# Performance work log

Hardware: AMD Instinct MI355X
Metric: run time of the kernel (lower is better)

## Reference

```python
import jax, jax.numpy as jnp
import numpy as np

B, W, G, E, NI, K = 2048, 8192, 8, 128, 16, 15


def setup_inputs() -> dict:
    key = jax.random.key(0)
    ks = jax.random.split(key, 12)
    wavelengths_nm = jnp.linspace(300.0, 400.0, W, dtype=jnp.float32)
    # Rayleigh optical depth (Hansen & Travis style approximation), AMF=1 column
    lam_um = wavelengths_nm / 1000.0
    rayleigh_od = (0.008569 * lam_um ** -4
                   * (1.0 + 0.0113 * lam_um ** -2 + 0.00013 * lam_um ** -4)).astype(jnp.float32)
    return {
        "gas_columns": jax.random.uniform(ks[0], (B, G), jnp.float32),
        "instrument_ids": jax.random.randint(ks[1], (B,), 0, NI),
        "nuisance_latent": jax.random.normal(ks[2], (B, G), jnp.float32),
        "air_mass": 1.0 + 2.0 * jax.random.uniform(ks[3], (B,), jnp.float32),
        "wavelengths_nm": wavelengths_nm,
        "absorption": 0.1 * jax.random.uniform(ks[4], (G, W), jnp.float32),
        "continuum_basis": 0.05 * jax.random.normal(ks[5], (G + 1, W), jnp.float32),
        "rayleigh_od": rayleigh_od,
        "embed_table": jax.random.normal(ks[6], (NI, E), jnp.float32),
        "w1": jax.random.normal(ks[7], (E + G, 64), jnp.float32) / np.sqrt(E + G),
        "b1": jnp.zeros((64,), jnp.float32),
        "w2": jax.random.normal(ks[8], (64, 7), jnp.float32) / 8.0,
        "b2": jnp.zeros((7,), jnp.float32),
    }


def _gaussian_kernel(width_px, kernel_size):
    half = (kernel_size - 1) / 2
    pos = jnp.linspace(-half, half, kernel_size, dtype=width_px.dtype)  # [K]
    k = jnp.exp(-0.5 * (pos[None, :] / (width_px[:, None] + 1e-6)) ** 2)  # [B,K]
    return k / k.sum(axis=1, keepdims=True)


def _forward(gas_columns, nuisance_latent, air_mass, wavelengths_nm, absorption,
             continuum_basis, rayleigh_od, embed_table, w1, b1, w2, b2,
             instrument_ids):
    b = gas_columns.shape[0]
    am = air_mass[:, None]                                   # [B,1]
    scaled = gas_columns * am                                # [B,G]
    optical_depth = scaled @ absorption                      # [B,W]
    ones = jnp.ones((b, 1), gas_columns.dtype)
    continuum = jnp.concatenate([gas_columns, ones], axis=1) @ continuum_basis  # [B,W]
    differential = optical_depth + continuum + am * rayleigh_od[None, :]

    # nuisance MLP on [latent, embedding]
    embed = embed_table[instrument_ids]                      # [B,E]
    nin = jnp.concatenate([nuisance_latent, embed], axis=-1)
    h = jax.nn.gelu(nin @ w1 + b1, approximate=False)
    p = h @ w2 + b2                                          # [B,7]

    gain = jax.nn.softplus(p[:, 0]) + 0.001
    offset = p[:, 1]
    woff = 0.05 * jnp.tanh(p[:, 2])
    wscale = 1.0 + 0.005 * jnp.tanh(p[:, 3])
    lsf = jnp.clip(jax.nn.softplus(p[:, 4]) + 0.001, 0.2, 5.0)
    stray = jax.nn.sigmoid(p[:, 5]) * 0.05
    nonlin = 0.02 * jnp.tanh(p[:, 6])

    # per-sample wavelength shift/scale + linear resampling
    new_wl = wavelengths_nm[None, :] * wscale[:, None] + woff[:, None]  # [B,W]
    differential = jax.vmap(lambda wq, d: jnp.interp(wq, wavelengths_nm, d))(new_wl, differential)

    # per-sample Gaussian LSF convolution (replicate padding)
    kernel = _gaussian_kernel(lsf, K)                        # [B,K]
    pad = K // 2
    padded = jnp.pad(differential, ((0, 0), (pad, pad)), mode='edge')  # [B,W+K-1]
    n = differential.shape[1]
    convolved = sum(padded[:, k:k + n] * kernel[:, k:k + 1] for k in range(K))

    counts = jnp.exp(-convolved)
    post = gain[:, None] * counts + offset[:, None]
    total_nl = jnp.clip(nonlin, -0.04, 0.04)                 # instrument nonlinearity = 0
    nl_counts = post + total_nl[:, None] * post ** 2
    total_stray = jnp.clip(stray, 0.0, 0.2)                  # instrument stray = 0
    simulated = (1.0 - total_stray[:, None]) * nl_counts \
        + total_stray[:, None] * nl_counts.mean(axis=1, keepdims=True)
    return simulated


def reference(gas_columns, instrument_ids, nuisance_latent, air_mass,
              wavelengths_nm, absorption, continuum_basis, rayleigh_od,
              embed_table, w1, b1, w2, b2):
    return _forward(gas_columns, nuisance_latent, air_mass, wavelengths_nm,
                    absorption, continuum_basis, rayleigh_od, embed_table,
                    w1, b1, w2, b2, instrument_ids)
```

## Files before the change

kernel.cpp:

```cpp
#include <hip/hip_runtime.h>

#define W_ 8192
#define NBATCH 2048
#define NT 256
#define NWAVE 4
#define SEGW 2048
#define CCH 256
#define NCHW 8
#define IRW 272

typedef unsigned short u16_t;
typedef _Float16 h2v __attribute__((ext_vector_type(2)));

__device__ __forceinline__ u16_t f2h(float x){ _Float16 h=(_Float16)x; return __builtin_bit_cast(u16_t,h); }
__device__ __forceinline__ float h2f(u16_t u){ return (float)__builtin_bit_cast(_Float16,u); }
__device__ __forceinline__ unsigned pk2(float a,float b){ return (unsigned)f2h(a)|((unsigned)f2h(b)<<16); }
__device__ __forceinline__ float dot2u(unsigned a,unsigned b,float c){
#if __has_builtin(__builtin_amdgcn_fdot2)
  return __builtin_amdgcn_fdot2(__builtin_bit_cast(h2v,a),__builtin_bit_cast(h2v,b),c,false);
#else
  h2v ha=__builtin_bit_cast(h2v,a), hb=__builtin_bit_cast(h2v,b);
  return c+(float)ha[0]*(float)hb[0]+(float)ha[1]*(float)hb[1];
#endif
}
__device__ __forceinline__ unsigned pkrtz(float a,float b){
#if __has_builtin(__builtin_amdgcn_cvt_pkrtz)
  return __builtin_bit_cast(unsigned, __builtin_amdgcn_cvt_pkrtz(a,b));
#else
  return pk2(a,b);
#endif
}
__device__ __forceinline__ unsigned alignb(unsigned hi, unsigned lo){
#if __has_builtin(__builtin_amdgcn_alignbit)
  return __builtin_amdgcn_alignbit(hi, lo, 16);
#else
  return (lo >> 16) | (hi << 16);
#endif
}
__device__ __forceinline__ float softplusf(float x){ return fmaxf(x,0.f)+log1pf(expf(-fabsf(x))); }
__device__ __forceinline__ unsigned rflv(unsigned v){
  return (unsigned)__builtin_amdgcn_readfirstlane((int)v);
}
__device__ __forceinline__ float rflvf(float v){
  return __builtin_bit_cast(float, __builtin_amdgcn_readfirstlane(__builtin_bit_cast(int, v)));
}

__global__ __launch_bounds__(256, 2)
void doas_pack(const float* __restrict__ absn, const float* __restrict__ cbn,
               const float* __restrict__ ray, unsigned* __restrict__ Tp){
  const int w = blockIdx.x*256 + threadIdx.x;
  #pragma unroll
  for (int q=0;q<4;++q) Tp[q*W_+w]     = pk2(absn[(2*q)*W_+w], absn[(2*q+1)*W_+w]);
  #pragma unroll
  for (int q=0;q<4;++q) Tp[(4+q)*W_+w] = pk2(cbn[(2*q)*W_+w],  cbn[(2*q+1)*W_+w]);
  Tp[8*W_+w] = pk2(cbn[8*W_+w], ray[w]);
}

template<bool CLO, bool CHI>
__device__ __forceinline__ void interp_chunk(int cbase, int l, const unsigned* __restrict__ rU,
                                             unsigned* __restrict__ irowU,
                                             float wscale, float posoff){
  #pragma unroll
  for (int it=0; it<3; ++it){
    const int pi = it*64 + l;
    if (pi < 136){
      float v2[2];
      #pragma unroll
      for (int u=0;u<2;++u){
        int j = cbase + 2*pi + u;
        if (CLO) j = max(j, 0);
        if (CHI) j = min(j, W_-1);
        float pos = fmaf((float)j, wscale, posoff);
        if (CLO) pos = fmaxf(pos, 0.0f);
        if (CHI) pos = fminf(pos, 8191.0f);
        int i0 = (int)pos;
        if (CHI) i0 = min(i0, W_-2);
        const float fr = pos - (float)i0;
        const int m = i0 >> 1;
        const unsigned u0 = rU[m];
        const unsigned u1 = rU[m+1];
        const unsigned hu0 = u0 >> 16;
        const bool odd = (i0 & 1);
        const unsigned ua = odd ? hu0 : u0;
        const unsigned ub = odd ? u1  : hu0;
        const float d0 = h2f((u16_t)ua);
        const float d1 = h2f((u16_t)ub);
        v2[u] = fmaf(fr, d1-d0, d0);
      }
      irowU[pi] = pkrtz(v2[0], v2[1]);
    }
  }
}

__global__ __launch_bounds__(NT, 2)
void doas_main9(const unsigned* __restrict__ Tp, const float* __restrict__ gas,
                const float* __restrict__ air, const int* __restrict__ iid,
                const float* __restrict__ nuis, const float* __restrict__ emb,
                const float* __restrict__ w1, const float* __restrict__ b1,
                const float* __restrict__ w2, const float* __restrict__ b2,
                float* __restrict__ out){
  __shared__ u16_t rowH[W_ + 16];
  __shared__ u16_t irowS[NWAVE][IRW];
  __shared__ float hS[64];
  __shared__ float pS[8];
  __shared__ float scalS[44];
  __shared__ float wsumS[NWAVE];

  const int tid = threadIdx.x;
  const int row = blockIdx.x;
  const int wid = tid >> 6, l = tid & 63;
  const int segbase = wid * SEGW;

  unsigned csg[9];
  {
    const float am = air[row];
    const float* gfp = gas + (size_t)row * 8;
    #pragma unroll
    for (int q=0;q<4;++q) csg[q]   = rflv(pk2(gfp[2*q]*am, gfp[2*q+1]*am));
    #pragma unroll
    for (int q=0;q<4;++q) csg[4+q] = rflv(pk2(gfp[2*q],    gfp[2*q+1]));
    csg[8] = rflv(pk2(1.0f, am));
  }

  unsigned* rowHU = (unsigned*)rowH;
  #pragma unroll
  for (int it=0; it<8; ++it){
    const int e0 = it*1024 + tid*4;
    uint4 dq[9];
    #pragma unroll
    for (int q=0;q<9;++q) dq[q] = *(const uint4*)(Tp + q*W_ + e0);
    float a0=0.f, a1=0.f, a2=0.f, a3=0.f;
    #pragma unroll
    for (int q=0;q<9;++q){
      a0 = dot2u(dq[q].x, csg[q], a0);
      a1 = dot2u(dq[q].y, csg[q], a1);
      a2 = dot2u(dq[q].z, csg[q], a2);
      a3 = dot2u(dq[q].w, csg[q], a3);
    }
    *(uint2*)(rowHU + (e0 >> 1)) = make_uint2(pkrtz(a0,a1), pkrtz(a2,a3));
  }

  if (tid < 64) {
    const int id = iid[row];
    float acc = b1[tid];
    const float* nrow = nuis + (size_t)row * 8;
    #pragma unroll
    for (int i = 0; i < 8; ++i) acc = fmaf(nrow[i], w1[i*64 + tid], acc);
    const float* erow = emb + (size_t)id * 128;
    #pragma unroll 8
    for (int i = 0; i < 128; ++i) acc = fmaf(erow[i], w1[(8+i)*64 + tid], acc);
    hS[tid] = 0.5f * acc * (1.0f + erff(acc * 0.70710678118654752f));
  }
  __syncthreads();
  if (tid < 7) {
    float p = b2[tid];
    for (int j = 0; j < 64; ++j) p = fmaf(hS[j], w2[j*7+tid], p);
    pS[tid] = p;
  }
  __syncthreads();
  if (tid == 0) {
    float p0=pS[0], p1=pS[1], p2=pS[2], p3=pS[3], p4=pS[4], p5=pS[5], p6=pS[6];
    float gainv = softplusf(p0) + 0.001f;
    float offv  = p1;
    float woffv = 0.05f * tanhf(p2);
    float wscv  = 1.0f + 0.005f * tanhf(p3);
    float lsf   = fminf(fmaxf(softplusf(p4) + 0.001f, 0.2f), 5.0f);
    float strv  = fminf(fmaxf((1.0f/(1.0f+expf(-p5))) * 0.05f, 0.0f), 0.2f);
    float nlin  = fminf(fmaxf(0.02f * tanhf(p6), -0.04f), 0.04f);
    float iw = 1.0f/(lsf + 1e-6f);
    float ks[15]; float ksum = 0.f;
    #pragma unroll
    for (int k2=0;k2<15;++k2){ float pp=(float)(k2-7)*iw; float e=expf(-0.5f*pp*pp); ks[k2]=e; ksum+=e; }
    float inv = 1.0f/ksum;
    unsigned* su = (unsigned*)scalS;
    #pragma unroll
    for (int i=0;i<7;++i) su[32+i] = pk2(ks[2*i]*inv, ks[2*i+1]*inv);
    su[39] = pk2(ks[14]*inv, 0.0f);
    scalS[15] = wscv;
    scalS[16] = (300.0f*(wscv - 1.0f) + woffv) * (8191.0f/100.0f);
    scalS[17] = gainv; scalS[18] = offv; scalS[19] = nlin; scalS[20] = strv;
  }
  __syncthreads();

  const unsigned* scalU = (const unsigned*)scalS;
  unsigned kwp[7];
  #pragma unroll
  for (int i=0;i<7;++i) kwp[i] = rflv(scalU[32+i]);
  const unsigned k14lo = rflv(scalU[39]);
  const float wscale = rflvf(scalS[15]), posoff = rflvf(scalS[16]);
  const float gainv  = rflvf(scalS[17]), offv   = rflvf(scalS[18]);
  const float nlin   = rflvf(scalS[19]), strv   = rflvf(scalS[20]);

  const unsigned* rU = (const unsigned*)rowH;
  u16_t* irow = &irowS[wid][0];
  unsigned* irowU = (unsigned*)irow;

  float accsum = 0.f;
  unsigned nlp[NCHW][2];

  #pragma unroll
  for (int c = 0; c < NCHW; ++c) {
    const int cs = segbase + c*CCH;
    const int cbase = cs - 8;
    if (wid == 0 && c == 0)
      interp_chunk<true,false>(cbase, l, rU, irowU, wscale, posoff);
    else if (wid == NWAVE-1 && c == NCHW-1)
      interp_chunk<false,true>(cbase, l, rU, irowU, wscale, posoff);
    else
      interp_chunk<false,false>(cbase, l, rU, irowU, wscale, posoff);
    __builtin_amdgcn_wave_barrier();
    {
      const uint2* p2 = (const uint2*)irowU + l;
      const uint2 A = p2[0], B = p2[1], C = p2[2], D = p2[3], E = p2[4];
      unsigned q[10] = {A.x,A.y, B.x,B.y, C.x,C.y, D.x,D.y, E.x,E.y};
      unsigned sh[9];
      #pragma unroll
      for (int m=0;m<9;++m) sh[m] = alignb(q[m+1], q[m]);
      float nlv[4];
      #pragma unroll
      for (int t=0;t<4;++t){
        float cv = 0.f;
        if ((t & 1) == 0){
          const int b0 = t >> 1;
          #pragma unroll
          for (int i=0;i<7;++i) cv = dot2u(sh[b0+i], kwp[i], cv);
          cv = dot2u(sh[b0+7], k14lo, cv);
        } else {
          const int b0 = (t+1) >> 1;
          #pragma unroll
          for (int i=0;i<7;++i) cv = dot2u(q[b0+i], kwp[i], cv);
          cv = dot2u(q[b0+7], k14lo, cv);
        }
        const float counts = __expf(-cv);
        const float post = fmaf(gainv, counts, offv);
        const float v = fmaf(nlin*post, post, post);
        accsum += v;
        nlv[t] = v;
      }
      nlp[c][0] = pkrtz(nlv[0], nlv[1]);
      nlp[c][1] = pkrtz(nlv[2], nlv[3]);
    }
    __builtin_amdgcn_wave_barrier();
  }

  float s = accsum;
  #pragma unroll
  for (int off2 = 32; off2 >= 1; off2 >>= 1) s += __shfl_down(s, off2);
  if (l == 0) wsumS[wid] = s;
  __syncthreads();
  const float meanv = (wsumS[0]+wsumS[1]+wsumS[2]+wsumS[3]) * (1.0f/8192.0f);

  {
    const float aa = 1.0f - strv;
    const float bb = strv * meanv;
    float* orow = out + (size_t)row * W_;
    #pragma unroll
    for (int c = 0; c < NCHW; ++c) {
      const unsigned u0 = nlp[c][0], u1 = nlp[c][1];
      float4 o0;
      o0.x = fmaf(aa, h2f((u16_t)(u0 & 0xffffu)), bb);
      o0.y = fmaf(aa, h2f((u16_t)(u0 >> 16)),     bb);
      o0.z = fmaf(aa, h2f((u16_t)(u1 & 0xffffu)), bb);
      o0.w = fmaf(aa, h2f((u16_t)(u1 >> 16)),     bb);
      *(float4*)(orow + segbase + c*CCH + 4*l) = o0;
    }
  }
}

__global__ __launch_bounds__(256, 2)
void doas_mono(const float* __restrict__ gas, const int* __restrict__ iid,
               const float* __restrict__ nuis, const float* __restrict__ air,
               const float* __restrict__ absn, const float* __restrict__ cbn,
               const float* __restrict__ ray, const float* __restrict__ emb,
               const float* __restrict__ w1, const float* __restrict__ b1,
               const float* __restrict__ w2, const float* __restrict__ b2,
               float* __restrict__ out)
{
  __shared__ u16_t ringS[4][2048];
  __shared__ u16_t irowS2[4][544];
  __shared__ float hS[64];
  __shared__ float pS[8];
  __shared__ float scalS[52];
  __shared__ float wsumS[4];

  const int tid = threadIdx.x;
  const int row = blockIdx.x;

  if (tid < 64) {
    const int j = tid;
    const int id = iid[row];
    float acc = b1[j];
    const float* nrow = nuis + (size_t)row * 8;
    #pragma unroll
    for (int i = 0; i < 8; ++i) acc = fmaf(nrow[i], w1[i*64 + j], acc);
    const float* erow = emb + (size_t)id * 128;
    for (int i = 0; i < 128; ++i) acc = fmaf(erow[i], w1[(8+i)*64 + j], acc);
    hS[j] = 0.5f * acc * (1.0f + erff(acc * 0.70710678118654752f));
  }
  __syncthreads();
  if (tid < 7) {
    float p = b2[tid];
    for (int j = 0; j < 64; ++j) p = fmaf(hS[j], w2[j*7+tid], p);
    pS[tid] = p;
  }
  __syncthreads();
  if (tid == 0) {
    float p0=pS[0], p1=pS[1], p2=pS[2], p3=pS[3], p4=pS[4], p5=pS[5], p6=pS[6];
    float gainv = softplusf(p0) + 0.001f;
    float offv  = p1;
    float woffv = 0.05f * tanhf(p2);
    float wscv  = 1.0f + 0.005f * tanhf(p3);
    float lsf   = fminf(fmaxf(softplusf(p4) + 0.001f, 0.2f), 5.0f);
    float strv  = fminf(fmaxf((1.0f/(1.0f+expf(-p5))) * 0.05f, 0.0f), 0.2f);
    float nlin  = fminf(fmaxf(0.02f * tanhf(p6), -0.04f), 0.04f);
    float iw = 1.0f/(lsf + 1e-6f);
    float ks[15]; float ksum = 0.f;
    #pragma unroll
    for (int k2=0;k2<15;++k2){ float pp=(float)(k2-7)*iw; float e=expf(-0.5f*pp*pp); ks[k2]=e; ksum+=e; }
    float inv = 1.0f/ksum;
    scalS[15] = wscv;
    scalS[16] = (300.0f*(wscv - 1.0f) + woffv) * (8191.0f/100.0f);
    scalS[17] = gainv; scalS[18] = offv; scalS[19] = nlin; scalS[20] = strv;
    scalS[22] = air[row];
    unsigned* su = (unsigned*)scalS;
    #pragma unroll
    for (int i=0;i<7;++i) su[32+i] = pk2(ks[2*i]*inv, ks[2*i+1]*inv);
    su[39] = pk2(ks[14]*inv, 0.0f);
    su[40] = pk2(0.0f, ks[14]*inv);
    #pragma unroll
    for (int g=0; g<8; ++g) scalS[23+g] = gas[(size_t)row*8+g];
  }
  __syncthreads();

  const int wid = tid >> 6, l = tid & 63;
  const int segbase = wid * 2048;
  const unsigned* scalU = (const unsigned*)scalS;
  unsigned kwp[7];
  #pragma unroll
  for (int i=0;i<7;++i) kwp[i] = rflv(scalU[32+i]);
  const unsigned k14lo = rflv(scalU[39]), k14hi = rflv(scalU[40]);
  const float wscale = scalS[15], posoff = scalS[16];
  const float gainv  = scalS[17], offv   = scalS[18];
  const float nlin   = scalS[19], strv   = scalS[20];

  u16_t* ring = &ringS[wid][0];
  unsigned* ringU = (unsigned*)ring;
  u16_t* irow = &irowS2[wid][0];
  unsigned* irowU = (unsigned*)irow;

  auto do_diff = [&](int s){
    const int sbase = segbase - 256 + (s << 9);
    #pragma unroll
    for (int it=0; it<4; ++it){
      const int e0 = sbase + ((it*64 + l) << 1);
      const int eL = min(max(e0, 0), W_-2);
      const float am = scalS[22];
      float a0=0.f, a1=0.f;
      #pragma unroll
      for (int g=0; g<8; ++g){
        const float cg = scalS[23+g];
        const float ca = cg*am;
        a0 = fmaf(ca, absn[g*W_+eL],   a0); a0 = fmaf(cg, cbn[g*W_+eL],   a0);
        a1 = fmaf(ca, absn[g*W_+eL+1], a1); a1 = fmaf(cg, cbn[g*W_+eL+1], a1);
      }
      a0 += cbn[8*W_+eL]   + am*ray[eL];
      a1 += cbn[8*W_+eL+1] + am*ray[eL+1];
      ringU[((unsigned)e0 & 2047) >> 1] = pkrtz(a0, a1);
    }
  };

  float accsum = 0.f;
  unsigned nlp[4][4];

  do_diff(0); do_diff(1);
  __builtin_amdgcn_wave_barrier();

  #pragma unroll
  for (int c = 0; c < 4; ++c) {
    if (c < 3) do_diff(c+2);
    __builtin_amdgcn_wave_barrier();
    {
      const int cbase = segbase + (c << 9) - 8;
      #pragma unroll
      for (int it = 0; it < 5; ++it) {
        const int pi = it*64 + l;
        if (pi < 264) {
          float v2[2];
          #pragma unroll
          for (int u=0; u<2; ++u){
            const int j = cbase + 2*pi + u;
            const int jc = min(max(j, 0), W_-1);
            float pos = fmaf((float)jc, wscale, posoff);
            pos = fminf(fmaxf(pos, 0.0f), 8191.0f);
            const int i0 = min((int)pos, W_-2);
            const float fr = pos - (float)i0;
            const float d0 = h2f(ring[ i0    & 2047]);
            const float d1 = h2f(ring[(i0+1) & 2047]);
            v2[u] = fmaf(fr, d1-d0, d0);
          }
          irowU[pi] = pkrtz(v2[0], v2[1]);
        }
      }
    }
    __builtin_amdgcn_wave_barrier();
    {
      const uint4* qp = (const uint4*)irow + l;
      const uint4 A = qp[0], B = qp[1], C = qp[2];
      unsigned q[12] = {A.x,A.y,A.z,A.w, B.x,B.y,B.z,B.w, C.x,C.y,C.z,C.w};
      unsigned sh[10];
      #pragma unroll
      for (int m=0;m<10;++m) sh[m] = alignb(q[m+1], q[m]);
      float nlv[8];
      #pragma unroll
      for (int t=0;t<8;++t){
        const int s2 = t >> 1;
        float cv = 0.f;
        if ((t & 1) == 0){
          #pragma unroll
          for (int i=0;i<7;++i) cv = dot2u(sh[s2+i], kwp[i], cv);
          cv = dot2u(q[s2+7], k14hi, cv);
        } else {
          #pragma unroll
          for (int i=0;i<7;++i) cv = dot2u(q[s2+1+i], kwp[i], cv);
          cv = dot2u(q[s2+8], k14lo, cv);
        }
        const float counts = __expf(-cv);
        const float post = fmaf(gainv, counts, offv);
        const float v = fmaf(nlin*post, post, post);
        accsum += v;
        nlv[t] = v;
      }
      nlp[c][0] = pkrtz(nlv[0], nlv[1]);
      nlp[c][1] = pkrtz(nlv[2], nlv[3]);
      nlp[c][2] = pkrtz(nlv[4], nlv[5]);
      nlp[c][3] = pkrtz(nlv[6], nlv[7]);
    }
    __builtin_amdgcn_wave_barrier();
  }

  float s = accsum;
  #pragma unroll
  for (int off2 = 32; off2 >= 1; off2 >>= 1) s += __shfl_down(s, off2);
  if (l == 0) wsumS[wid] = s;
  __syncthreads();
  const float meanv = (wsumS[0]+wsumS[1]+wsumS[2]+wsumS[3]) * (1.0f/8192.0f);

  {
    const float aa = 1.0f - strv;
    const float bb = strv * meanv;
    float* orow = out + (size_t)row * W_;
    #pragma unroll
    for (int c = 0; c < 4; ++c) {
      const unsigned u0 = nlp[c][0], u1 = nlp[c][1], u2 = nlp[c][2], u3 = nlp[c][3];
      float4 o0, o1;
      o0.x = fmaf(aa, h2f((u16_t)(u0 & 0xffffu)), bb);
      o0.y = fmaf(aa, h2f((u16_t)(u0 >> 16)),     bb);
      o0.z = fmaf(aa, h2f((u16_t)(u1 & 0xffffu)), bb);
      o0.w = fmaf(aa, h2f((u16_t)(u1 >> 16)),     bb);
      o1.x = fmaf(aa, h2f((u16_t)(u2 & 0xffffu)), bb);
      o1.y = fmaf(aa, h2f((u16_t)(u2 >> 16)),     bb);
      o1.z = fmaf(aa, h2f((u16_t)(u3 & 0xffffu)), bb);
      o1.w = fmaf(aa, h2f((u16_t)(u3 >> 16)),     bb);
      float* dst = orow + segbase + (c << 9) + 8*l;
      *(float4*)(dst)     = o0;
      *(float4*)(dst + 4) = o1;
    }
  }
}

extern "C" void kernel_launch(void* const* d_in, const int* in_sizes, int n_in,
                              void* d_out, int out_size, void* d_ws, size_t ws_size,
                              hipStream_t stream) {
  const float* gas  = (const float*)d_in[0];
  const int*   iid  = (const int*)d_in[1];
  const float* nuis = (const float*)d_in[2];
  const float* air  = (const float*)d_in[3];
  const float* wl   = (const float*)d_in[4];
  const float* absn = (const float*)d_in[5];
  const float* cbn  = (const float*)d_in[6];
  const float* ray  = (const float*)d_in[7];
  const float* emb  = (const float*)d_in[8];
  const float* w1   = (const float*)d_in[9];
  const float* b1   = (const float*)d_in[10];
  const float* w2   = (const float*)d_in[11];
  const float* b2   = (const float*)d_in[12];
  float* out = (float*)d_out;
  (void)in_sizes; (void)n_in; (void)out_size; (void)wl;

  const size_t packBytes = (size_t)9 * W_ * 4;

  if (ws_size >= packBytes) {
    unsigned* Tp = (unsigned*)d_ws;
    hipLaunchKernelGGL(doas_pack, dim3(W_/256), dim3(256), 0, stream, absn, cbn, ray, Tp);
    hipLaunchKernelGGL(doas_main9, dim3(NBATCH), dim3(NT), 0, stream,
                       Tp, gas, air, iid, nuis, emb, w1, b1, w2, b2, out);
  } else {
    hipLaunchKernelGGL(doas_mono, dim3(NBATCH), dim3(256), 0, stream,
                       gas, iid, nuis, air, absn, cbn, ray, emb, w1, b1, w2, b2, out);
  }
}
```

Before: 60.65 us.

## Specialize warps: three build spectrum row while fourth runs nuisance MLP

Splits the block by wavefront. Wavefronts 0-2 compute the optical-depth row (now 11 iterations of 768 elements, with a bounds check). Wavefront 3 concurrently computes the nuisance MLP and reduces the second layer with wave shuffles instead of shared memory. This removes two block-wide barriers and the serial second-layer loop, overlapping the MLP with the row build. The cost is that the row build runs on three wavefronts instead of four, and the last iteration is partially masked.

```diff
diff --git a/kernel.cpp b/kernel.cpp
--- a/kernel.cpp
+++ b/kernel.cpp
@@ -93,16 +93,14 @@
 }
 
 __global__ __launch_bounds__(NT, 2)
-void doas_main9(const unsigned* __restrict__ Tp, const float* __restrict__ gas,
-                const float* __restrict__ air, const int* __restrict__ iid,
-                const float* __restrict__ nuis, const float* __restrict__ emb,
-                const float* __restrict__ w1, const float* __restrict__ b1,
-                const float* __restrict__ w2, const float* __restrict__ b2,
-                float* __restrict__ out){
+void doas_main11(const unsigned* __restrict__ Tp, const float* __restrict__ gas,
+                 const float* __restrict__ air, const int* __restrict__ iid,
+                 const float* __restrict__ nuis, const float* __restrict__ emb,
+                 const float* __restrict__ w1, const float* __restrict__ b1,
+                 const float* __restrict__ w2, const float* __restrict__ b2,
+                 float* __restrict__ out){
   __shared__ u16_t rowH[W_ + 16];
   __shared__ u16_t irowS[NWAVE][IRW];
-  __shared__ float hS[64];
-  __shared__ float pS[8];
   __shared__ float scalS[44];
   __shared__ float wsumS[NWAVE];
 
@@ -111,74 +109,83 @@
   const int wid = tid >> 6, l = tid & 63;
   const int segbase = wid * SEGW;
 
-  unsigned csg[9];
-  {
-    const float am = air[row];
-    const float* gfp = gas + (size_t)row * 8;
-    #pragma unroll
-    for (int q=0;q<4;++q) csg[q]   = rflv(pk2(gfp[2*q]*am, gfp[2*q+1]*am));
-    #pragma unroll
-    for (int q=0;q<4;++q) csg[4+q] = rflv(pk2(gfp[2*q],    gfp[2*q+1]));
-    csg[8] = rflv(pk2(1.0f, am));
-  }
-
-  unsigned* rowHU = (unsigned*)rowH;
-  #pragma unroll
-  for (int it=0; it<8; ++it){
-    const int e0 = it*1024 + tid*4;
-    uint4 dq[9];
-    #pragma unroll
-    for (int q=0;q<9;++q) dq[q] = *(const uint4*)(Tp + q*W_ + e0);
-    float a0=0.f, a1=0.f, a2=0.f, a3=0.f;
-    #pragma unroll
-    for (int q=0;q<9;++q){
-      a0 = dot2u(dq[q].x, csg[q], a0);
-      a1 = dot2u(dq[q].y, csg[q], a1);
-      a2 = dot2u(dq[q].z, csg[q], a2);
-      a3 = dot2u(dq[q].w, csg[q], a3);
-    }
-    *(uint2*)(rowHU + (e0 >> 1)) = make_uint2(pkrtz(a0,a1), pkrtz(a2,a3));
-  }
-
-  if (tid < 64) {
-    const int id = iid[row];
-    float acc = b1[tid];
-    const float* nrow = nuis + (size_t)row * 8;
-    #pragma unroll
-    for (int i = 0; i < 8; ++i) acc = fmaf(nrow[i], w1[i*64 + tid], acc);
-    const float* erow = emb + (size_t)id * 128;
-    #pragma unroll 8
-    for (int i = 0; i < 128; ++i) acc = fmaf(erow[i], w1[(8+i)*64 + tid], acc);
-    hS[tid] = 0.5f * acc * (1.0f + erff(acc * 0.70710678118654752f));
-  }
-  __syncthreads();
-  if (tid < 7) {
-    float p = b2[tid];
-    for (int j = 0; j < 64; ++j) p = fmaf(hS[j], w2[j*7+tid], p);
-    pS[tid] = p;
-  }
-  __syncthreads();
-  if (tid == 0) {
-    float p0=pS[0], p1=pS[1], p2=pS[2], p3=pS[3], p4=pS[4], p5=pS[5], p6=pS[6];
-    float gainv = softplusf(p0) + 0.001f;
-    float offv  = p1;
-    float woffv = 0.05f * tanhf(p2);
-    float wscv  = 1.0f + 0.005f * tanhf(p3);
-    float lsf   = fminf(fmaxf(softplusf(p4) + 0.001f, 0.2f), 5.0f);
-    float strv  = fminf(fmaxf((1.0f/(1.0f+expf(-p5))) * 0.05f, 0.0f), 0.2f);
-    float nlin  = fminf(fmaxf(0.02f * tanhf(p6), -0.04f), 0.04f);
-    float iw = 1.0f/(lsf + 1e-6f);
-    float ks[15]; float ksum = 0.f;
-    #pragma unroll
-    for (int k2=0;k2<15;++k2){ float pp=(float)(k2-7)*iw; float e=expf(-0.5f*pp*pp); ks[k2]=e; ksum+=e; }
-    float inv = 1.0f/ksum;
-    unsigned* su = (unsigned*)scalS;
-    #pragma unroll
-    for (int i=0;i<7;++i) su[32+i] = pk2(ks[2*i]*inv, ks[2*i+1]*inv);
-    su[39] = pk2(ks[14]*inv, 0.0f);
-    scalS[15] = wscv;
-    scalS[16] = (300.0f*(wscv - 1.0f) + woffv) * (8191.0f/100.0f);
-    scalS[17] = gainv; scalS[18] = offv; scalS[19] = nlin; scalS[20] = strv;
+  if (wid < 3){
+    unsigned csg[9];
+    {
+      const float am = air[row];
+      const float* gfp = gas + (size_t)row * 8;
+      #pragma unroll
+      for (int q=0;q<4;++q) csg[q]   = rflv(pk2(gfp[2*q]*am, gfp[2*q+1]*am));
+      #pragma unroll
+      for (int q=0;q<4;++q) csg[4+q] = rflv(pk2(gfp[2*q],    gfp[2*q+1]));
+      csg[8] = rflv(pk2(1.0f, am));
+    }
+    unsigned* rowHU = (unsigned*)rowH;
+    #pragma unroll
+    for (int it=0; it<11; ++it){
+      const int e0 = it*768 + tid*4;
+      if (e0 < W_){
+        uint4 dq[9];
+        #pragma unroll
+        for (int q=0;q<9;++q) dq[q] = *(const uint4*)(Tp + q*W_ + e0);
+        float a0=0.f, a1=0.f, a2=0.f, a3=0.f;
+        #pragma unroll
+        for (int q=0;q<9;++q){
+          a0 = dot2u(dq[q].x, csg[q], a0);
+          a1 = dot2u(dq[q].y, csg[q], a1);
+          a2 = dot2u(dq[q].z, csg[q], a2);
+          a3 = dot2u(dq[q].w, csg[q], a3);
+        }
+        *(uint2*)(rowHU + (e0 >> 1)) = make_uint2(pkrtz(a0,a1), pkrtz(a2,a3));
+      }
+    }
+  } else {
+    float hj;
+    {
+      const int id = iid[row];
+      float acc = b1[l];
+      const float* nrow = nuis + (size_t)row * 8;
+      #pragma unroll
+      for (int i = 0; i < 8; ++i) acc = fmaf(nrow[i], w1[i*64 + l], acc);
+      const float* erow = emb + (size_t)id * 128;
+      #pragma unroll 8
+      for (int i = 0; i < 128; ++i) acc = fmaf(erow[i], w1[(8+i)*64 + l], acc);
+      hj = 0.5f * acc * (1.0f + erff(acc * 0.70710678118654752f));
+    }
+    float pv[7];
+    {
+      const float* w2r = w2 + l*7;
+      #pragma unroll
+      for (int k=0;k<7;++k) pv[k] = hj * w2r[k];
+      #pragma unroll
+      for (int off=32; off>=1; off>>=1){
+        #pragma unroll
+        for (int k=0;k<7;++k) pv[k] += __shfl_down(pv[k], off);
+      }
+    }
+    if (l == 0){
+      float p0=pv[0]+b2[0], p1=pv[1]+b2[1], p2=pv[2]+b2[2], p3=pv[3]+b2[3],
+            p4=pv[4]+b2[4], p5=pv[5]+b2[5], p6=pv[6]+b2[6];
+      float gainv = softplusf(p0) + 0.001f;
+      float offv  = p1;
+      float woffv = 0.05f * tanhf(p2);
+      float wscv  = 1.0f + 0.005f * tanhf(p3);
+      float lsf   = fminf(fmaxf(softplusf(p4) + 0.001f, 0.2f), 5.0f);
+      float strv  = fminf(fmaxf((1.0f/(1.0f+expf(-p5))) * 0.05f, 0.0f), 0.2f);
+      float nlin  = fminf(fmaxf(0.02f * tanhf(p6), -0.04f), 0.04f);
+      float iw = 1.0f/(lsf + 1e-6f);
+      float ks[15]; float ksum = 0.f;
+      #pragma unroll
+      for (int k2=0;k2<15;++k2){ float pp=(float)(k2-7)*iw; float e=expf(-0.5f*pp*pp); ks[k2]=e; ksum+=e; }
+      float inv = 1.0f/ksum;
+      unsigned* su = (unsigned*)scalS;
+      #pragma unroll
+      for (int i=0;i<7;++i) su[32+i] = pk2(ks[2*i]*inv, ks[2*i+1]*inv);
+      su[39] = pk2(ks[14]*inv, 0.0f);
+      scalS[15] = wscv;
+      scalS[16] = (300.0f*(wscv - 1.0f) + woffv) * (8191.0f/100.0f);
+      scalS[17] = gainv; scalS[18] = offv; scalS[19] = nlin; scalS[20] = strv;
+    }
   }
   __syncthreads();
 
@@ -492,7 +499,7 @@
   if (ws_size >= packBytes) {
     unsigned* Tp = (unsigned*)d_ws;
     hipLaunchKernelGGL(doas_pack, dim3(W_/256), dim3(256), 0, stream, absn, cbn, ray, Tp);
-    hipLaunchKernelGGL(doas_main9, dim3(NBATCH), dim3(NT), 0, stream,
+    hipLaunchKernelGGL(doas_main11, dim3(NBATCH), dim3(NT), 0, stream,
                        Tp, gas, air, iid, nuis, emb, w1, b1, w2, b2, out);
   } else {
     hipLaunchKernelGGL(doas_mono, dim3(NBATCH), dim3(256), 0, stream,
```

Measured after the change: 53.68 us. -11.5%, faster.
